# Performance work log

Hardware: AMD Instinct MI355X
Metric: run time of the kernel (lower is better)

## Reference

```python
import jax, jax.numpy as jnp
import numpy as np

L, H, E, DK, FF, V, BS = 6, 16, 1024, 64, 4096, 32000, 1024
B, T = 2, 1024
EPS = 1e-5


def _ln(x, g, b):
    mu = jnp.mean(x, axis=-1, keepdims=True)
    var = jnp.mean(jnp.square(x - mu), axis=-1, keepdims=True)
    return (x - mu) * jax.lax.rsqrt(var + EPS) * g + b


def setup_inputs() -> dict:
    key = jax.random.key(0)
    ks = jax.random.split(key, 12)
    s = 0.02
    return {
        'idx': jax.random.randint(ks[0], (B, T), 0, V),
        'emb': jax.random.normal(ks[1], (V, E), jnp.float32) * s,
        'pos': jax.random.normal(ks[2], (BS, E), jnp.float32) * s,
        'Wq': jax.random.normal(ks[3], (L, H, E, DK), jnp.float32) * s,
        'Wk': jax.random.normal(ks[4], (L, H, E, DK), jnp.float32) * s,
        'Wv': jax.random.normal(ks[5], (L, H, E, DK), jnp.float32) * s,
        'Wp': jax.random.normal(ks[6], (L, E, E), jnp.float32) * s,
        'bp': jnp.zeros((L, E), jnp.float32),
        'ln1_g': jnp.ones((L, E), jnp.float32),
        'ln1_b': jnp.zeros((L, E), jnp.float32),
        'ln2_g': jnp.ones((L, E), jnp.float32),
        'ln2_b': jnp.zeros((L, E), jnp.float32),
        'W1': jax.random.normal(ks[7], (L, E, FF), jnp.float32) * s,
        'b1': jnp.zeros((L, FF), jnp.float32),
        'W2': jax.random.normal(ks[8], (L, FF, E), jnp.float32) * s,
        'b2': jnp.zeros((L, E), jnp.float32),
        'lnf_g': jnp.ones((E,), jnp.float32),
        'lnf_b': jnp.zeros((E,), jnp.float32),
        'Wout': jax.random.normal(ks[9], (E, V), jnp.float32) * s,
        'bout': jnp.zeros((V,), jnp.float32),
    }


def reference(idx, emb, pos, Wq, Wk, Wv, Wp, bp, ln1_g, ln1_b, ln2_g, ln2_b,
              W1, b1, W2, b2, lnf_g, lnf_b, Wout, bout):
    Tcur = idx.shape[1]
    x = emb[idx] + pos[:Tcur]  # [B,T,E]
    # NOTE: original code scales by 1/sqrt(n_embd) (input dim), NOT 1/sqrt(d_k)
    scale = 1.0 / jnp.sqrt(jnp.float32(E))
    causal = jnp.tril(jnp.ones((Tcur, Tcur), bool))
    neg_inf = jnp.float32(-jnp.inf)
    for l in range(L):
        h = _ln(x, ln1_g[l], ln1_b[l])
        q = jnp.einsum('bte,hed->bhtd', h, Wq[l])
        k = jnp.einsum('bte,hed->bhtd', h, Wk[l])
        v = jnp.einsum('bte,hed->bhtd', h, Wv[l])
        scores = jnp.einsum('bhtd,bhsd->bhts', q, k) * scale
        scores = jnp.where(causal, scores, neg_inf)
        attn = jax.nn.softmax(scores, axis=-1)
        o = jnp.einsum('bhts,bhsd->bhtd', attn, v)
        o = o.transpose(0, 2, 1, 3).reshape(x.shape[0], Tcur, H * DK)
        x = x + o @ Wp[l] + bp[l]
        h = _ln(x, ln2_g[l], ln2_b[l])
        x = x + jax.nn.relu(h @ W1[l] + b1[l]) @ W2[l] + b2[l]
    x = _ln(x, lnf_g, lnf_b)
    logits = x @ Wout + bout  # [B,T,V]
    return logits
```

## Files before the change

kernel.cpp:

```cpp
#include <hip/hip_runtime.h>
#include <cstdio>
#include <cstdint>

typedef unsigned short u16;
typedef __bf16 bf16x8 __attribute__((ext_vector_type(8)));
typedef float f32x4 __attribute__((ext_vector_type(4)));

static const int EE = 1024;
static const int TT = 1024;
static const int BB = 2;
static const int NTOK = 2048;
static const int HH = 16;
static const int DK = 64;
static const int FF = 4096;
static const int VV = 32000;
static const int LL = 6;

__device__ __forceinline__ float bf2f(u16 u) {
  unsigned int i = ((unsigned int)u) << 16;
  float f; __builtin_memcpy(&f, &i, 4); return f;
}
__device__ __forceinline__ u16 f2bf(float f) {
  unsigned int i; __builtin_memcpy(&i, &f, 4);
  unsigned int r = i + 0x7fffu + ((i >> 16) & 1u);
  return (u16)(r >> 16);
}

__device__ __forceinline__ void gll16(const u16* g, u16* l) {
  __builtin_amdgcn_global_load_lds(
      (__attribute__((address_space(1))) void*)(uintptr_t)g,
      (__attribute__((address_space(3))) void*)l,
      16, 0, 0);
}

__global__ __launch_bounds__(256) void embed_k(const int* __restrict__ idx,
                                               const float* __restrict__ emb,
                                               const float* __restrict__ pos,
                                               float* __restrict__ x) {
  long i = (long)blockIdx.x * 256 + threadIdx.x;
  int n = (int)(i >> 10), e = (int)(i & 1023);
  int tok = idx[n];
  int t = n & (TT - 1);
  x[i] = emb[(long)tok * EE + e] + pos[(long)t * EE + e];
}

template <int NS>
__global__ __launch_bounds__(256) void ln_fused_k(float* __restrict__ x,
                                                  const u16* __restrict__ part, long pstride,
                                                  const float* __restrict__ bias,
                                                  const float* __restrict__ g,
                                                  const float* __restrict__ b,
                                                  u16* __restrict__ out) {
  int row = blockIdx.x * 4 + (threadIdx.x >> 6);
  int lane = threadIdx.x & 63;
  long base = (long)row * EE;
  float v[16];
  float s = 0.f, s2 = 0.f;
#pragma unroll
  for (int j = 0; j < 16; j++) {
    int c = j * 64 + lane;
    float t = x[base + c];
    if constexpr (NS > 0) {
      t += bias[c];
#pragma unroll
      for (int p = 0; p < NS; p++) t += bf2f(part[(long)p * pstride + base + c]);
      x[base + c] = t;
    }
    v[j] = t; s += t; s2 += t * t;
  }
#pragma unroll
  for (int o = 32; o; o >>= 1) { s += __shfl_xor(s, o); s2 += __shfl_xor(s2, o); }
  float mu = s * (1.f / EE);
  float var = s2 * (1.f / EE) - mu * mu;
  float rs = rsqrtf(var + 1e-5f);
  u16* orow = out + base;
#pragma unroll
  for (int j = 0; j < 16; j++) {
    int c = j * 64 + lane;
    orow[c] = f2bf((v[j] - mu) * rs * g[c] + b[c]);
  }
}

__global__ __launch_bounds__(256) void pack_qkvT_k(const float* __restrict__ Wq,
                                                   const float* __restrict__ Wk,
                                                   const float* __restrict__ Wv,
                                                   u16* __restrict__ out) {
  int l = blockIdx.y;
  const float* Wq_l = Wq + (size_t)l * HH * EE * DK;
  const float* Wk_l = Wk + (size_t)l * HH * EE * DK;
  const float* Wv_l = Wv + (size_t)l * HH * EE * DK;
  u16* out_l = out + (size_t)l * 3 * EE * EE;
  long base = ((long)blockIdx.x * 256 + threadIdx.x) * 4;
  int c = (int)(base >> 10);
  int e0 = (int)(base & 1023);
  const float* W = (c < 1024) ? Wq_l : (c < 2048 ? Wk_l : Wv_l);
  int cm = c & 1023;
  int hh = cm >> 6, d = cm & 63;
#pragma unroll
  for (int i = 0; i < 4; i++) {
    int e = e0 + i;
    out_l[(long)c * EE + e] = f2bf(W[((long)hh * EE + e) * DK + d]);
  }
}

template <typename ST>
__global__ __launch_bounds__(256) void transpose_to_bf16(const ST* __restrict__ src,
                                                         long s_z1, long s_z2, int zmod, int ld_s,
                                                         u16* __restrict__ dst,
                                                         long d_z, int ld_d, int R, int C) {
  __shared__ u16 t[32][33];
  int z = blockIdx.z;
  const ST* S = src + (z / zmod) * s_z1 + (z % zmod) * s_z2;
  u16* D = dst + (long)z * d_z;
  int c0 = blockIdx.x * 32, r0 = blockIdx.y * 32;
  int lx = threadIdx.x & 31, ly = threadIdx.x >> 5;
#pragma unroll
  for (int i = 0; i < 4; i++) {
    int r = r0 + ly + i * 8;
    ST val = S[(long)r * ld_s + c0 + lx];
    if constexpr (sizeof(ST) == 4) t[ly + i * 8][lx] = f2bf((float)val);
    else t[ly + i * 8][lx] = (u16)val;
  }
  __syncthreads();
#pragma unroll
  for (int i = 0; i < 4; i++) {
    int c = c0 + ly + i * 8;
    D[(long)c * ld_d + r0 + lx] = t[lx][ly + i * 8];
  }
}

__global__ __launch_bounds__(256) void flash_attn_k(const u16* __restrict__ qkv,
                                                    const u16* __restrict__ vT,
                                                    u16* __restrict__ o) {
  __shared__ u16 Qs[64 * 72];
  __shared__ u16 Ks[2][64 * 72];
  __shared__ u16 Vs[2][64 * 72];
  __shared__ u16 Ps[4][16 * 72];

  int tid = threadIdx.x;
  int lane = tid & 63, w = tid >> 6;
  int fr = lane & 15, kg = lane >> 4;
  int z = blockIdx.y;
  int b = z >> 4, h = z & 15;
  const u16* qbase = qkv + (long)b * TT * 3072 + h * 64;
  const u16* kbase = qbase + 1024;
  const u16* vbase = vT + (long)z * DK * TT;
  const float scale = 0.03125f;

  for (int p = 0; p < 2; p++) {
    int jq = (p == 0) ? (int)blockIdx.x : 15 - (int)blockIdx.x;
    int q0 = jq * 64;
    int nt = jq + 1;
    if (p) __syncthreads();

    int4 kreg[2], vreg[2];
#pragma unroll
    for (int i = 0; i < 2; i++) {
      int c = i * 256 + tid, row = c >> 3, c8 = c & 7;
      *(int4*)&Qs[row * 72 + c8 * 8] = *(const int4*)(qbase + (long)(q0 + row) * 3072 + c8 * 8);
      kreg[i] = *(const int4*)(kbase + (long)row * 3072 + c8 * 8);
      vreg[i] = *(const int4*)(vbase + (long)row * TT + c8 * 8);
    }
#pragma unroll
    for (int i = 0; i < 2; i++) {
      int c = i * 256 + tid, row = c >> 3, c8 = c & 7;
      *(int4*)&Ks[0][row * 72 + c8 * 8] = kreg[i];
      *(int4*)&Vs[0][row * 72 + c8 * 8] = vreg[i];
    }
    __syncthreads();

    f32x4 zero = {0.f, 0.f, 0.f, 0.f};
    f32x4 acc_o[4];
    float m_i[4], l_i[4];
#pragma unroll
    for (int n = 0; n < 4; n++) acc_o[n] = zero;
#pragma unroll
    for (int r = 0; r < 4; r++) { m_i[r] = -1e30f; l_i[r] = 0.f; }

    for (int t = 0; t < nt; t++) {
      int cur = t & 1;
      int kv0 = t * 64;
      bool pf = (t + 1 < nt);
      if (pf) {
        int kvn = kv0 + 64;
#pragma unroll
        for (int i = 0; i < 2; i++) {
          int c = i * 256 + tid, row = c >> 3, c8 = c & 7;
          kreg[i] = *(const int4*)(kbase + (long)(kvn + row) * 3072 + c8 * 8);
          vreg[i] = *(const int4*)(vbase + (long)row * TT + kvn + c8 * 8);
        }
      }

      f32x4 s[4];
#pragma unroll
      for (int n = 0; n < 4; n++) s[n] = zero;
      {
        bf16x8 aq[2], bk[4][2];
#pragma unroll
        for (int kk = 0; kk < 2; kk++)
          aq[kk] = *(const bf16x8*)&Qs[(w * 16 + fr) * 72 + kk * 32 + kg * 8];
#pragma unroll
        for (int n = 0; n < 4; n++)
#pragma unroll
          for (int kk = 0; kk < 2; kk++)
            bk[n][kk] = *(const bf16x8*)&Ks[cur][(n * 16 + fr) * 72 + kk * 32 + kg * 8];
#pragma unroll
        for (int kk = 0; kk < 2; kk++)
#pragma unroll
          for (int n = 0; n < 4; n++)
            s[n] = __builtin_amdgcn_mfma_f32_16x16x32_bf16(aq[kk], bk[n][kk], s[n], 0, 0, 0);
      }

      float sv[4][4];
#pragma unroll
      for (int n = 0; n < 4; n++)
#pragma unroll
        for (int r = 0; r < 4; r++) {
          int qg = q0 + w * 16 + kg * 4 + r;
          int kgl = kv0 + n * 16 + fr;
          float val = s[n][r] * scale;
          sv[n][r] = (kgl > qg) ? -1e30f : val;
        }
#pragma unroll
      for (int r = 0; r < 4; r++) {
        float rm = fmaxf(fmaxf(sv[0][r], sv[1][r]), fmaxf(sv[2][r], sv[3][r]));
        rm = fmaxf(rm, __shfl_xor(rm, 1));
        rm = fmaxf(rm, __shfl_xor(rm, 2));
        rm = fmaxf(rm, __shfl_xor(rm, 4));
        rm = fmaxf(rm, __shfl_xor(rm, 8));
        float mn = fmaxf(m_i[r], rm);
        float f = __expf(m_i[r] - mn);
        m_i[r] = mn;
        float rs = 0.f;
#pragma unroll
        for (int n = 0; n < 4; n++) {
          float pv = __expf(sv[n][r] - mn);
          sv[n][r] = pv;
          rs += pv;
        }
        rs += __shfl_xor(rs, 1);
        rs += __shfl_xor(rs, 2);
        rs += __shfl_xor(rs, 4);
        rs += __shfl_xor(rs, 8);
        l_i[r] = l_i[r] * f + rs;
#pragma unroll
        for (int n = 0; n < 4; n++) acc_o[n][r] *= f;
      }
#pragma unroll
      for (int n = 0; n < 4; n++)
#pragma unroll
        for (int r = 0; r < 4; r++)
          Ps[w][(kg * 4 + r) * 72 + n * 16 + fr] = f2bf(sv[n][r]);

      {
        bf16x8 pa[2], bv[4][2];
#pragma unroll
        for (int kk = 0; kk < 2; kk++)
          pa[kk] = *(const bf16x8*)&Ps[w][fr * 72 + kk * 32 + kg * 8];
#pragma unroll
        for (int n = 0; n < 4; n++)
#pragma unroll
          for (int kk = 0; kk < 2; kk++)
            bv[n][kk] = *(const bf16x8*)&Vs[cur][(n * 16 + fr) * 72 + kk * 32 + kg * 8];
#pragma unroll
        for (int kk = 0; kk < 2; kk++)
#pragma unroll
          for (int n = 0; n < 4; n++)
            acc_o[n] = __builtin_amdgcn_mfma_f32_16x16x32_bf16(pa[kk], bv[n][kk], acc_o[n], 0, 0, 0);
      }

      if (pf) {
#pragma unroll
        for (int i = 0; i < 2; i++) {
          int c = i * 256 + tid, row = c >> 3, c8 = c & 7;
          *(int4*)&Ks[cur ^ 1][row * 72 + c8 * 8] = kreg[i];
          *(int4*)&Vs[cur ^ 1][row * 72 + c8 * 8] = vreg[i];
        }
      }
      __syncthreads();
    }

    u16* obase = o + ((long)b * TT + q0) * EE + h * 64;
#pragma unroll
    for (int r = 0; r < 4; r++) {
      float inv = 1.f / l_i[r];
      int qrow = w * 16 + kg * 4 + r;
#pragma unroll
      for (int n = 0; n < 4; n++)
        obase[(long)qrow * EE + n * 16 + fr] = f2bf(acc_o[n][r] * inv);
    }
  }
}

template <int EPI>
__global__ __launch_bounds__(256) void gemm_nt(
    const u16* __restrict__ A, const u16* __restrict__ BT, void* Cv,
    const float* __restrict__ bias,
    int Kc, int lda, int ldb, int ldc, long c_zs) {
  constexpr int BK = 64;
  __shared__ u16 As[2][128 * BK];
  __shared__ u16 Bs[2][128 * BK];

  int m0 = blockIdx.x * 128, n0 = blockIdx.y * 128;
  int z = blockIdx.z;
  int tid = threadIdx.x, lane = tid & 63, wave = tid >> 6;
  int wm = wave >> 1, wn = wave & 1;
  int fr = lane & 15, kg = lane >> 4;
  int xk0 = ((kg) ^ (fr & 7)) * 8;
  int xk1 = ((4 + kg) ^ (fr & 7)) * 8;
  int kbeg = z * Kc;

  auto STAGE = [&](int t, int b) {
    int k0 = kbeg + t * BK;
#pragma unroll
    for (int i = 0; i < 4; i++) {
      int c = i * 256 + tid, row = c >> 3;
      int ch = (c & 7) ^ (row & 7);
      gll16(A + (long)(m0 + row) * lda + k0 + ch * 8, &As[b][c * 8]);
      gll16(BT + (long)(n0 + row) * ldb + k0 + ch * 8, &Bs[b][c * 8]);
    }
  };

  f32x4 zero = {0.f, 0.f, 0.f, 0.f};
  f32x4 acc[4][4];
#pragma unroll
  for (int m = 0; m < 4; m++)
#pragma unroll
    for (int n = 0; n < 4; n++) acc[m][n] = zero;

  int NT = Kc / BK;
  STAGE(0, 0);
  if (NT > 1) STAGE(1, 1);

  for (int c = 0; c < NT; c++) {
    if (c + 1 < NT) asm volatile("s_waitcnt vmcnt(8)" ::: "memory");
    else            asm volatile("s_waitcnt vmcnt(0)" ::: "memory");
    __builtin_amdgcn_s_barrier();
    const u16* Ab = As[c & 1];
    const u16* Bb = Bs[c & 1];
#pragma unroll
    for (int kk = 0; kk < 2; kk++) {
      int xo = kk ? xk1 : xk0;
      bf16x8 af[4], bf[4];
#pragma unroll
      for (int m = 0; m < 4; m++)
        af[m] = *(const bf16x8*)&Ab[(wm * 64 + m * 16 + fr) * BK + xo];
#pragma unroll
      for (int n = 0; n < 4; n++)
        bf[n] = *(const bf16x8*)&Bb[(wn * 64 + n * 16 + fr) * BK + xo];
      __builtin_amdgcn_s_setprio(1);
#pragma unroll
      for (int m = 0; m < 4; m++)
#pragma unroll
        for (int n = 0; n < 4; n++)
          acc[m][n] = __builtin_amdgcn_mfma_f32_16x16x32_bf16(af[m], bf[n], acc[m][n], 0, 0, 0);
      __builtin_amdgcn_s_setprio(0);
    }
    __builtin_amdgcn_s_barrier();
    if (c + 2 < NT) STAGE(c + 2, c & 1);
  }

  u16* C16 = (u16*)Cv;
  float* C32 = (float*)Cv;
  long cb = (long)z * c_zs;
  int rowb = m0 + wm * 64, colb = n0 + wn * 64;
#pragma unroll
  for (int m = 0; m < 4; m++) {
#pragma unroll
    for (int n = 0; n < 4; n++) {
      int gc = colb + n * 16 + fr;
      float bv = 0.f;
      if (EPI == 1 || EPI == 2) bv = bias[gc];
#pragma unroll
      for (int r = 0; r < 4; r++) {
        int gr = rowb + m * 16 + kg * 4 + r;
        long ci = cb + (long)gr * ldc + gc;
        float val = acc[m][n][r];
        if (EPI == 0) C16[ci] = f2bf(val);
        else if (EPI == 1) C32[ci] = val + bv;
        else if (EPI == 2) C16[ci] = f2bf(fmaxf(val + bv, 0.f));
        else C16[ci] = f2bf(val);
      }
    }
  }
}

__global__ __launch_bounds__(512) void gemm256_nt(
    const u16* __restrict__ A, const u16* __restrict__ BT,
    float* __restrict__ C, const float* __restrict__ bias,
    int K, int lda, int ldb, int ldc) {
  __shared__ u16 lds[2][2][256 * 64];

  int tid = threadIdx.x, lane = tid & 63, wave = tid >> 6;
  int wm = wave >> 2, wn = wave & 3;
  int fr = lane & 15, kg = lane >> 4;
  int m0 = blockIdx.x * 256, n0 = blockIdx.y * 256;

  auto STAGE = [&](int t, int b) {
    int k0 = t * 64;
#pragma unroll
    for (int r = 0; r < 4; r++) {
      int g = r * 512 + tid;
      int row = g >> 3, cl = (g & 7) ^ (row & 7);
      gll16(A + (long)(m0 + row) * lda + k0 + cl * 8, &lds[b][0][g * 8]);
    }
#pragma unroll
    for (int r = 0; r < 4; r++) {
      int g = r * 512 + tid;
      int row = g >> 3, cl = (g & 7) ^ (row & 7);
      gll16(BT + (long)(n0 + row) * ldb + k0 + cl * 8, &lds[b][1][g * 8]);
    }
  };

  f32x4 zero = {0.f, 0.f, 0.f, 0.f};
  f32x4 acc[8][4];
#pragma unroll
  for (int m = 0; m < 8; m++)
#pragma unroll
    for (int n = 0; n < 4; n++) acc[m][n] = zero;

  int NT = K / 64;
  STAGE(0, 0);
  if (NT > 1) STAGE(1, 1);

  for (int c = 0; c < NT; c++) {
    if (c + 1 < NT) asm volatile("s_waitcnt vmcnt(8)" ::: "memory");
    else            asm volatile("s_waitcnt vmcnt(0)" ::: "memory");
    __builtin_amdgcn_s_barrier();
    const u16* Ab = lds[c & 1][0];
    const u16* Bb = lds[c & 1][1];
#pragma unroll
    for (int ph = 0; ph < 4; ph++) {
      int mh = ph >> 1, nh = ph & 1;
      bf16x8 af[4][2], bf[2][2];
#pragma unroll
      for (int m = 0; m < 4; m++) {
        int row = wm * 128 + mh * 64 + m * 16 + fr;
#pragma unroll
        for (int kk = 0; kk < 2; kk++) {
          int cp = (kk * 4 + kg) ^ (row & 7);
          af[m][kk] = *(const bf16x8*)&Ab[row * 64 + cp * 8];
        }
      }
#pragma unroll
      for (int n = 0; n < 2; n++) {
        int row = wn * 64 + nh * 32 + n * 16 + fr;
#pragma unroll
        for (int kk = 0; kk < 2; kk++) {
          int cp = (kk * 4 + kg) ^ (row & 7);
          bf[n][kk] = *(const bf16x8*)&Bb[row * 64 + cp * 8];
        }
      }
      __builtin_amdgcn_s_setprio(1);
#pragma unroll
      for (int kk = 0; kk < 2; kk++)
#pragma unroll
        for (int m = 0; m < 4; m++)
#pragma unroll
          for (int n = 0; n < 2; n++)
            acc[mh * 4 + m][nh * 2 + n] = __builtin_amdgcn_mfma_f32_16x16x32_bf16(
                af[m][kk], bf[n][kk], acc[mh * 4 + m][nh * 2 + n], 0, 0, 0);
      __builtin_amdgcn_s_setprio(0);
    }
    __builtin_amdgcn_s_barrier();
    if (c + 2 < NT) STAGE(c + 2, c & 1);
  }

  int rowb = m0 + wm * 128, colb = n0 + wn * 64;
#pragma unroll
  for (int m = 0; m < 8; m++) {
#pragma unroll
    for (int n = 0; n < 4; n++) {
      int gc = colb + n * 16 + fr;
      float bv = bias[gc];
#pragma unroll
      for (int r = 0; r < 4; r++) {
        int gr = rowb + m * 16 + kg * 4 + r;
        C[(long)gr * ldc + gc] = acc[m][n][r] + bv;
      }
    }
  }
}

extern "C" void kernel_launch(void* const* d_in, const int* in_sizes, int n_in,
                              void* d_out, int out_size, void* d_ws, size_t ws_size,
                              hipStream_t stream) {
  const int*   idx  = (const int*)d_in[0];
  const float* emb  = (const float*)d_in[1];
  const float* pos  = (const float*)d_in[2];
  const float* Wq   = (const float*)d_in[3];
  const float* Wk   = (const float*)d_in[4];
  const float* Wv   = (const float*)d_in[5];
  const float* Wp   = (const float*)d_in[6];
  const float* bp   = (const float*)d_in[7];
  const float* ln1g = (const float*)d_in[8];
  const float* ln1b = (const float*)d_in[9];
  const float* ln2g = (const float*)d_in[10];
  const float* ln2b = (const float*)d_in[11];
  const float* W1   = (const float*)d_in[12];
  const float* b1   = (const float*)d_in[13];
  const float* W2   = (const float*)d_in[14];
  const float* b2   = (const float*)d_in[15];
  const float* lnfg = (const float*)d_in[16];
  const float* lnfb = (const float*)d_in[17];
  const float* Wout = (const float*)d_in[18];
  const float* bout = (const float*)d_in[19];

  char* w = (char*)d_ws;
  size_t off = 0;
  auto alloc = [&](size_t bytes) {
    void* p = w + off;
    off += (bytes + 255) & ~(size_t)255;
    return p;
  };
  float* x    = (float*)alloc((size_t)NTOK * EE * 4);
  u16* h      = (u16*)alloc((size_t)NTOK * EE * 2);
  u16* qkv    = (u16*)alloc((size_t)NTOK * 3 * EE * 2);
  u16* vT     = (u16*)alloc((size_t)BB * HH * DK * TT * 2);
  u16* big    = (u16*)alloc((size_t)VV * EE * 2);
  u16* o      = (u16*)alloc((size_t)NTOK * EE * 2);
  u16* mid    = (u16*)alloc((size_t)NTOK * FF * 2);
  u16* W1T    = (u16*)alloc((size_t)FF * EE * 2);
  u16* W2T    = (u16*)alloc((size_t)EE * FF * 2);
  u16* pbuf   = (u16*)alloc((size_t)4 * NTOK * EE * 2);
  if (off > ws_size) {
    fprintf(stderr, "kernel_launch: ws too small, need %zu have %zu\n", off, ws_size);
    return;
  }
  size_t off_saved = off;
  u16* W1T_all = (u16*)alloc((size_t)LL * FF * EE * 2);
  u16* W2T_all = (u16*)alloc((size_t)LL * EE * FF * 2);
  bool hoist = (off <= ws_size);
  if (!hoist) off = off_saved;

  u16* WqkvT_all = big;
  u16* WpT_all   = big + (size_t)6 * 3 * EE * EE;
  const long PS = (long)NTOK * EE;

  embed_k<<<NTOK * EE / 256, 256, 0, stream>>>(idx, emb, pos, x);
  pack_qkvT_k<<<dim3(3 * EE * EE / 1024, LL), 256, 0, stream>>>(Wq, Wk, Wv, WqkvT_all);
  transpose_to_bf16<float><<<dim3(32, 32, LL), 256, 0, stream>>>(
      Wp, (long)EE * EE, 0, 1, EE, WpT_all, (long)EE * EE, EE, EE, EE);
  if (hoist) {
    transpose_to_bf16<float><<<dim3(FF / 32, EE / 32, LL), 256, 0, stream>>>(
        W1, (long)EE * FF, 0, 1, FF, W1T_all, (long)FF * EE, EE, EE, FF);
    transpose_to_bf16<float><<<dim3(EE / 32, FF / 32, LL), 256, 0, stream>>>(
        W2, (long)FF * EE, 0, 1, EE, W2T_all, (long)EE * FF, FF, FF, EE);
  }

  for (int l = 0; l < LL; l++) {
    if (l == 0)
      ln_fused_k<0><<<NTOK / 4, 256, 0, stream>>>(x, nullptr, 0, nullptr,
                                                  ln1g, ln1b, h);
    else
      ln_fused_k<4><<<NTOK / 4, 256, 0, stream>>>(x, pbuf, PS, b2 + (l - 1) * EE,
                                                  ln1g + l * EE, ln1b + l * EE, h);
    gemm_nt<0><<<dim3(16, 24, 1), 256, 0, stream>>>(
        h, WqkvT_all + (size_t)l * 3 * EE * EE, qkv, nullptr,
        EE, EE, EE, 3 * EE, 0);
    transpose_to_bf16<u16><<<dim3(2, 32, 32), 256, 0, stream>>>(
        qkv + 2 * EE, (long)TT * 3 * EE, 64, 16, 3 * EE,
        vT, (long)DK * TT, TT, TT, DK);
    flash_attn_k<<<dim3(8, 32), 256, 0, stream>>>(qkv, vT, o);
    gemm_nt<4><<<dim3(16, 8, 2), 256, 0, stream>>>(
        o, WpT_all + (size_t)l * EE * EE, pbuf, nullptr,
        512, EE, EE, EE, PS);
    ln_fused_k<2><<<NTOK / 4, 256, 0, stream>>>(x, pbuf, PS, bp + l * EE,
                                                ln2g + l * EE, ln2b + l * EE, h);
    const u16* w1t = hoist ? (W1T_all + (size_t)l * FF * EE) : W1T;
    if (!hoist)
      transpose_to_bf16<float><<<dim3(FF / 32, EE / 32, 1), 256, 0, stream>>>(
          W1 + (size_t)l * EE * FF, 0, 0, 1, FF, W1T, 0, EE, EE, FF);
    gemm_nt<2><<<dim3(16, 32, 1), 256, 0, stream>>>(
        h, w1t, mid, b1 + l * FF,
        EE, EE, EE, FF, 0);
    const u16* w2t = hoist ? (W2T_all + (size_t)l * EE * FF) : W2T;
    if (!hoist)
      transpose_to_bf16<float><<<dim3(EE / 32, FF / 32, 1), 256, 0, stream>>>(
          W2 + (size_t)l * FF * EE, 0, 0, 1, EE, W2T, 0, FF, FF, EE);
    gemm_nt<4><<<dim3(16, 8, 4), 256, 0, stream>>>(
        mid, w2t, pbuf, nullptr,
        1024, FF, FF, EE, PS);
  }

  ln_fused_k<4><<<NTOK / 4, 256, 0, stream>>>(x, pbuf, PS, b2 + 5 * EE, lnfg, lnfb, h);
  u16* WoutT = big;
  transpose_to_bf16<float><<<dim3(VV / 32, EE / 32, 1), 256, 0, stream>>>(
      Wout, 0, 0, 1, VV, WoutT, 0, EE, EE, VV);
  gemm256_nt<<<dim3(NTOK / 256, VV / 256, 1), 512, 0, stream>>>(
      h, WoutT, (float*)d_out, bout, EE, EE, EE, VV);
}
```

Baseline: 1.311 ms.

## Restructure LM-head GEMM into 8-phase schedule with interleaved half-tile loads

Rewrites the 256x256 output-projection GEMM so each K-tile is split into four compute phases, each covering a quadrant of the block tile. Global-to-LDS loads are issued one half-operand at a time, spread across those phases, with barriers and vmcnt waits between them. The wave-to-quadrant mapping also changes so each wave owns a 64x32 sub-tile in every quadrant. The aim is finer overlap of memory traffic with MFMA work, at the cost of extra barriers per K-tile and more complex wait accounting.

```diff
diff --git a/kernel.cpp b/kernel.cpp
--- a/kernel.cpp
+++ b/kernel.cpp
@@ -385,98 +385,134 @@
   }
 }
 
-__global__ __launch_bounds__(512) void gemm256_nt(
+__global__ __launch_bounds__(512) void gemm256_8p(
     const u16* __restrict__ A, const u16* __restrict__ BT,
     float* __restrict__ C, const float* __restrict__ bias,
     int K, int lda, int ldb, int ldc) {
   __shared__ u16 lds[2][2][256 * 64];
 
   int tid = threadIdx.x, lane = tid & 63, wave = tid >> 6;
-  int wm = wave >> 2, wn = wave & 3;
+  int wr = wave >> 2, wc = wave & 3;
   int fr = lane & 15, kg = lane >> 4;
   int m0 = blockIdx.x * 256, n0 = blockIdx.y * 256;
 
-  auto STAGE = [&](int t, int b) {
+  auto STAGEH = [&](int t, int sh) {
+    int op = sh & 1, half = sh >> 1;
+    const u16* src = op ? BT : A;
+    int ld = op ? ldb : lda;
+    int gb = op ? n0 : m0;
     int k0 = t * 64;
-#pragma unroll
-    for (int r = 0; r < 4; r++) {
+    int b = t & 1;
+#pragma unroll
+    for (int r = 0; r < 2; r++) {
       int g = r * 512 + tid;
-      int row = g >> 3, cl = (g & 7) ^ (row & 7);
-      gll16(A + (long)(m0 + row) * lda + k0 + cl * 8, &lds[b][0][g * 8]);
-    }
-#pragma unroll
-    for (int r = 0; r < 4; r++) {
-      int g = r * 512 + tid;
-      int row = g >> 3, cl = (g & 7) ^ (row & 7);
-      gll16(BT + (long)(n0 + row) * ldb + k0 + cl * 8, &lds[b][1][g * 8]);
+      int rl = g >> 3, c8 = g & 7;
+      int row = half * 128 + rl;
+      int cl = c8 ^ (row & 7);
+      gll16(src + (long)(gb + row) * ld + k0 + cl * 8,
+            &lds[b][op][row * 64 + c8 * 8]);
     }
   };
 
   f32x4 zero = {0.f, 0.f, 0.f, 0.f};
-  f32x4 acc[8][4];
-#pragma unroll
-  for (int m = 0; m < 8; m++)
-#pragma unroll
-    for (int n = 0; n < 4; n++) acc[m][n] = zero;
+  f32x4 acc[4][4][2];
+#pragma unroll
+  for (int q = 0; q < 4; q++)
+#pragma unroll
+    for (int m = 0; m < 4; m++)
+#pragma unroll
+      for (int n = 0; n < 2; n++) acc[q][m][n] = zero;
 
   int NT = K / 64;
-  STAGE(0, 0);
-  if (NT > 1) STAGE(1, 1);
-
-  for (int c = 0; c < NT; c++) {
-    if (c + 1 < NT) asm volatile("s_waitcnt vmcnt(8)" ::: "memory");
-    else            asm volatile("s_waitcnt vmcnt(0)" ::: "memory");
-    __builtin_amdgcn_s_barrier();
-    const u16* Ab = lds[c & 1][0];
-    const u16* Bb = lds[c & 1][1];
-#pragma unroll
-    for (int ph = 0; ph < 4; ph++) {
-      int mh = ph >> 1, nh = ph & 1;
-      bf16x8 af[4][2], bf[2][2];
-#pragma unroll
-      for (int m = 0; m < 4; m++) {
-        int row = wm * 128 + mh * 64 + m * 16 + fr;
-#pragma unroll
-        for (int kk = 0; kk < 2; kk++) {
-          int cp = (kk * 4 + kg) ^ (row & 7);
-          af[m][kk] = *(const bf16x8*)&Ab[row * 64 + cp * 8];
-        }
-      }
+#pragma unroll
+  for (int sh = 0; sh < 4; sh++) STAGEH(0, sh);
+  if (NT > 1) {
+#pragma unroll
+    for (int sh = 0; sh < 4; sh++) STAGEH(1, sh);
+  }
+
+  for (int tc = 0; tc < NT; tc++) {
+    const u16* Ab = lds[tc & 1][0];
+    const u16* Bb = lds[tc & 1][1];
+#pragma unroll
+    for (int q = 0; q < 4; q++) {
+      const int mh = q >> 1, nh = q & 1;
+      int P = 4 * tc + q;
+      int st = (P + 6) >> 2, sh = (P + 6) & 3;
+      bool issue = (st >= 2 && st < NT);
+      bf16x8 af[4][2], bfr[2][2];
+
+      if (q == 0) {
+        if (issue) STAGEH(st, sh);
+        if (tc == 0) {
+          if (NT > 1) asm volatile("s_waitcnt vmcnt(8)" ::: "memory");
+          else        asm volatile("s_waitcnt vmcnt(0)" ::: "memory");
+        } else if (tc + 1 < NT) {
+          asm volatile("s_waitcnt vmcnt(6)" ::: "memory");
+        } else {
+          asm volatile("s_waitcnt vmcnt(0)" ::: "memory");
+        }
+        __builtin_amdgcn_s_barrier();
+#pragma unroll
+        for (int m = 0; m < 4; m++) {
+          int row = mh * 128 + wr * 64 + m * 16 + fr;
+          af[m][0] = *(const bf16x8*)&Ab[row * 64 + ((kg) ^ (row & 7)) * 8];
+          af[m][1] = *(const bf16x8*)&Ab[row * 64 + ((4 + kg) ^ (row & 7)) * 8];
+        }
+#pragma unroll
+        for (int n = 0; n < 2; n++) {
+          int row = nh * 128 + wc * 32 + n * 16 + fr;
+          bfr[n][0] = *(const bf16x8*)&Bb[row * 64 + ((kg) ^ (row & 7)) * 8];
+          bfr[n][1] = *(const bf16x8*)&Bb[row * 64 + ((4 + kg) ^ (row & 7)) * 8];
+        }
+      } else {
+#pragma unroll
+        for (int m = 0; m < 4; m++) {
+          int row = mh * 128 + wr * 64 + m * 16 + fr;
+          af[m][0] = *(const bf16x8*)&Ab[row * 64 + ((kg) ^ (row & 7)) * 8];
+          af[m][1] = *(const bf16x8*)&Ab[row * 64 + ((4 + kg) ^ (row & 7)) * 8];
+        }
+#pragma unroll
+        for (int n = 0; n < 2; n++) {
+          int row = nh * 128 + wc * 32 + n * 16 + fr;
+          bfr[n][0] = *(const bf16x8*)&Bb[row * 64 + ((kg) ^ (row & 7)) * 8];
+          bfr[n][1] = *(const bf16x8*)&Bb[row * 64 + ((4 + kg) ^ (row & 7)) * 8];
+        }
+        if (issue) STAGEH(st, sh);
+        __builtin_amdgcn_s_barrier();
+      }
+      asm volatile("s_waitcnt lgkmcnt(0)" ::: "memory");
+      __builtin_amdgcn_sched_barrier(0);
+      __builtin_amdgcn_s_setprio(1);
+#pragma unroll
+      for (int kk = 0; kk < 2; kk++)
+#pragma unroll
+        for (int m = 0; m < 4; m++)
+#pragma unroll
+          for (int n = 0; n < 2; n++)
+            acc[q][m][n] = __builtin_amdgcn_mfma_f32_16x16x32_bf16(
+                af[m][kk], bfr[n][kk], acc[q][m][n], 0, 0, 0);
+      __builtin_amdgcn_s_setprio(0);
+      __builtin_amdgcn_s_barrier();
+    }
+  }
+
+#pragma unroll
+  for (int q = 0; q < 4; q++) {
+    const int mh = q >> 1, nh = q & 1;
+    int rowb = m0 + mh * 128 + wr * 64;
+    int colb = n0 + nh * 128 + wc * 32;
+#pragma unroll
+    for (int m = 0; m < 4; m++) {
 #pragma unroll
       for (int n = 0; n < 2; n++) {
-        int row = wn * 64 + nh * 32 + n * 16 + fr;
-#pragma unroll
-        for (int kk = 0; kk < 2; kk++) {
-          int cp = (kk * 4 + kg) ^ (row & 7);
-          bf[n][kk] = *(const bf16x8*)&Bb[row * 64 + cp * 8];
-        }
-      }
-      __builtin_amdgcn_s_setprio(1);
-#pragma unroll
-      for (int kk = 0; kk < 2; kk++)
-#pragma unroll
-        for (int m = 0; m < 4; m++)
-#pragma unroll
-          for (int n = 0; n < 2; n++)
-            acc[mh * 4 + m][nh * 2 + n] = __builtin_amdgcn_mfma_f32_16x16x32_bf16(
-                af[m][kk], bf[n][kk], acc[mh * 4 + m][nh * 2 + n], 0, 0, 0);
-      __builtin_amdgcn_s_setprio(0);
-    }
-    __builtin_amdgcn_s_barrier();
-    if (c + 2 < NT) STAGE(c + 2, c & 1);
-  }
-
-  int rowb = m0 + wm * 128, colb = n0 + wn * 64;
-#pragma unroll
-  for (int m = 0; m < 8; m++) {
-#pragma unroll
-    for (int n = 0; n < 4; n++) {
-      int gc = colb + n * 16 + fr;
-      float bv = bias[gc];
-#pragma unroll
-      for (int r = 0; r < 4; r++) {
-        int gr = rowb + m * 16 + kg * 4 + r;
-        C[(long)gr * ldc + gc] = acc[m][n][r] + bv;
+        int gc = colb + n * 16 + fr;
+        float bv = bias[gc];
+#pragma unroll
+        for (int r = 0; r < 4; r++) {
+          int gr = rowb + m * 16 + kg * 4 + r;
+          C[(long)gr * ldc + gc] = acc[q][m][n][r] + bv;
+        }
       }
     }
   }
@@ -587,6 +623,6 @@
   u16* WoutT = big;
   transpose_to_bf16<float><<<dim3(VV / 32, EE / 32, 1), 256, 0, stream>>>(
       Wout, 0, 0, 1, VV, WoutT, 0, EE, EE, VV);
-  gemm256_nt<<<dim3(NTOK / 256, VV / 256, 1), 512, 0, stream>>>(
+  gemm256_8p<<<dim3(NTOK / 256, VV / 256, 1), 512, 0, stream>>>(
       h, WoutT, (float*)d_out, bout, EE, EE, EE, VV);
 }
```

After: 1.320 ms. No clear change (+0.7%).
